# Optimization experiments

Hardware: AMD Instinct MI355X
Metric: run time of the kernel (lower is better)

## Reference

```python
import jax, jax.numpy as jnp
import numpy as np

B, S, D = 2, 2048, 1024
H, HD = 16, 64  # num_heads, head_dim
EPS = 1e-6      # flax LayerNorm default
ROPE_BASE = 10000.0


def _layernorm(x, scale, bias=None, eps=EPS):
    mu = jnp.mean(x, axis=-1, keepdims=True)
    var = jnp.mean(jnp.square(x - mu), axis=-1, keepdims=True)
    y = (x - mu) * jax.lax.rsqrt(var + eps) * scale
    return y + bias if bias is not None else y


def _rotate_half(x):
    x1, x2 = x[..., : x.shape[-1] // 2], x[..., x.shape[-1] // 2 :]
    return jnp.concatenate((-x2, x1), axis=-1)


def _rope_tables(seq_len, head_dim, dtype):
    inv_freq = 1.0 / ROPE_BASE ** (jnp.arange(0, head_dim, 2, dtype=jnp.float32) / head_dim)
    t = jnp.arange(seq_len, dtype=jnp.float32)
    freqs = jnp.einsum('i,j->ij', t, inv_freq)          # [S, HD/2]
    emb = jnp.concatenate((freqs, freqs), axis=-1)      # [S, HD]
    return jnp.cos(emb).astype(dtype), jnp.sin(emb).astype(dtype)


def setup_inputs() -> dict:
    key = jax.random.key(0)
    ks = jax.random.split(key, 4)
    return {
        'x': jax.random.normal(ks[0], (B, S, D), dtype=jnp.float32),
        'w_qkv': jax.random.normal(ks[1], (D, 3 * D), dtype=jnp.float32) * (1.0 / np.sqrt(D)),
        'b_qkv': jnp.zeros((3 * D,), dtype=jnp.float32),
        'w_out': jax.random.normal(ks[2], (D, D), dtype=jnp.float32) * (0.1 / np.sqrt(D)),
        'b_out': jnp.zeros((D,), dtype=jnp.float32),
        'ln_scale': jnp.ones((D,), dtype=jnp.float32),
        'ln_bias': jnp.zeros((D,), dtype=jnp.float32),
        'q_scale': jnp.ones((HD,), dtype=jnp.float32),
        'k_scale': jnp.ones((HD,), dtype=jnp.float32),
    }


def reference(x, w_qkv, b_qkv, w_out, b_out, ln_scale, ln_bias, q_scale, k_scale):
    b, s, d = x.shape
    # input LayerNorm
    xn = _layernorm(x, ln_scale, ln_bias)
    # fused QKV projection
    qkv = xn @ w_qkv + b_qkv                              # [B, S, 3D]
    q, k, v = jnp.split(qkv, 3, axis=-1)
    def to_bhsd(t):
        return t.reshape(b, s, H, HD).transpose(0, 2, 1, 3)
    q, k, v = to_bhsd(q), to_bhsd(k), to_bhsd(v)          # [B, H, S, HD]
    # per-head QK LayerNorm (no bias)
    q = _layernorm(q, q_scale)
    k = _layernorm(k, k_scale)
    # RoPE
    cos, sin = _rope_tables(s, HD, q.dtype)               # [S, HD]
    cos, sin = cos[None, None], sin[None, None]
    q = q * cos + _rotate_half(q) * sin
    k = k * cos + _rotate_half(k) * sin
    # scaled dot-product attention (softmax over key positions)
    scale = 1.0 / np.sqrt(HD)
    scores = jnp.einsum('bhqd,bhkd->bhqk', q, k) * scale  # [B, H, S, S]
    probs = jax.nn.softmax(scores, axis=-1)
    attn = jnp.einsum('bhqk,bhkd->bhqd', probs, v)        # [B, H, S, HD]
    attn = attn.transpose(0, 2, 1, 3).reshape(b, s, d)
    return attn @ w_out + b_out
```

## Files before the change

kernel.cpp:

```cpp
#include <hip/hip_runtime.h>
#include <math.h>

#define BB 2
#define SS 2048
#define DD 1024
#define HH 16
#define HDD 64
static constexpr float EPS = 1e-6f;

typedef __bf16 bf16x8 __attribute__((ext_vector_type(8)));
typedef __bf16 bf16x4 __attribute__((ext_vector_type(4)));
typedef float f32x4 __attribute__((ext_vector_type(4)));
typedef __attribute__((address_space(1))) const unsigned int gas_u32;
typedef __attribute__((address_space(3))) unsigned int las_u32;

__device__ __forceinline__ unsigned short f2bf(float f) {
    unsigned int u = __float_as_uint(f);
    u = (u + 0x7FFFu + ((u >> 16) & 1u)) >> 16;
    return (unsigned short)u;
}

__device__ __forceinline__ uint2 pack4bf(float a, float b, float c, float d) {
    bf16x4 v;
    v[0] = (__bf16)a; v[1] = (__bf16)b; v[2] = (__bf16)c; v[3] = (__bf16)d;
    return *(uint2*)&v;
}

__device__ __forceinline__ void async_ld16(const unsigned short* g, unsigned short* l) {
    __builtin_amdgcn_global_load_lds((gas_u32*)g, (las_u32*)l, 16, 0, 0);
}

__global__ __launch_bounds__(256) void cast_transpose(const float* __restrict__ w,
                                                      unsigned short* __restrict__ wt,
                                                      int K, int N) {
    __shared__ float tile[32][36];
    const int n0 = blockIdx.x * 32;
    const int k0 = blockIdx.y * 32;
    const int t = threadIdx.x;
    const int r = t >> 3;
    const int c = (t & 7) * 4;
    *(float4*)&tile[r][c] = *(const float4*)(w + (size_t)(k0 + r) * N + n0 + c);
    __syncthreads();
    unsigned short o[4];
#pragma unroll
    for (int i = 0; i < 4; i++) o[i] = f2bf(tile[c + i][r]);
    *(uint2*)(wt + (size_t)(n0 + r) * K + k0 + c) = *(uint2*)o;
}

__global__ __launch_bounds__(256) void rope_tables(float* __restrict__ ctab,
                                                   float* __restrict__ stab) {
    const int idx = blockIdx.x * 256 + threadIdx.x;
    const int s = idx >> 5;
    const int i = idx & 31;
    const float ang = (float)s * exp2f(-(float)i * (13.287712379549449f / 32.f));
    ctab[idx] = cosf(ang);
    stab[idx] = sinf(ang);
}

__global__ __launch_bounds__(256) void ln_kernel(const float* __restrict__ x,
                                                 const float* __restrict__ scale,
                                                 const float* __restrict__ bias,
                                                 unsigned short* __restrict__ xn) {
    __shared__ float red[4];
    const int row = blockIdx.x;
    const int t = threadIdx.x;
    const float* xr = x + (size_t)row * DD + t * 4;

    float4 v = *(const float4*)xr;
    float s = v.x + v.y + v.z + v.w;
#pragma unroll
    for (int o = 32; o; o >>= 1) s += __shfl_xor(s, o);
    if ((t & 63) == 0) red[t >> 6] = s;
    __syncthreads();
    const float mu = (red[0] + red[1] + red[2] + red[3]) * (1.f / DD);

    float4 d = {v.x - mu, v.y - mu, v.z - mu, v.w - mu};
    float sq = d.x * d.x + d.y * d.y + d.z * d.z + d.w * d.w;
#pragma unroll
    for (int o = 32; o; o >>= 1) sq += __shfl_xor(sq, o);
    __syncthreads();
    if ((t & 63) == 0) red[t >> 6] = sq;
    __syncthreads();
    const float var = (red[0] + red[1] + red[2] + red[3]) * (1.f / DD);
    const float rstd = rsqrtf(var + EPS);

    const float4 sc = *(const float4*)(scale + t * 4);
    const float4 bi = *(const float4*)(bias + t * 4);
    unsigned short o[4];
    o[0] = f2bf(d.x * rstd * sc.x + bi.x);
    o[1] = f2bf(d.y * rstd * sc.y + bi.y);
    o[2] = f2bf(d.z * rstd * sc.z + bi.z);
    o[3] = f2bf(d.w * rstd * sc.w + bi.w);
    *(uint2*)(xn + (size_t)row * DD + t * 4) = *(uint2*)o;
}

__global__ __launch_bounds__(256) void gemm_mfma_bt(const unsigned short* __restrict__ A,
                                                    const unsigned short* __restrict__ Bt,
                                                    const float* __restrict__ bias,
                                                    float* __restrict__ C,
                                                    int M, int N, int K) {
    __shared__ __align__(16) unsigned short As[128][32];
    __shared__ __align__(16) unsigned short Bs[128][32];

    const int bm = blockIdx.y * 128;
    const int bn = blockIdx.x * 128;
    const int t = threadIdx.x;
    const int wv = t >> 6;
    const int ln = t & 63;
    const int m16 = ln & 15;
    const int quad = ln >> 4;
    const int wm = (wv >> 1) * 64;
    const int wn = (wv & 1) * 64;

    f32x4 acc[4][4];
#pragma unroll
    for (int i = 0; i < 4; i++)
#pragma unroll
        for (int j = 0; j < 4; j++) acc[i][j] = (f32x4){0.f, 0.f, 0.f, 0.f};

    const int srow = wv * 32 + (ln >> 2);
    const int sk = (ln & 3) * 8;
    const unsigned short* aptr = A + (size_t)(bm + srow) * K + sk;
    const unsigned short* bptr = Bt + (size_t)(bn + srow) * K + sk;
    unsigned short* al0 = &As[wv * 32][0];
    unsigned short* al1 = &As[wv * 32 + 16][0];
    unsigned short* bl0 = &Bs[wv * 32][0];
    unsigned short* bl1 = &Bs[wv * 32 + 16][0];

    for (int k0 = 0; k0 < K; k0 += 32) {
        __syncthreads();
        async_ld16(aptr, al0);
        async_ld16(aptr + 16 * (size_t)K, al1);
        async_ld16(bptr, bl0);
        async_ld16(bptr + 16 * (size_t)K, bl1);
        __syncthreads();

        bf16x8 af[4], bf[4];
#pragma unroll
        for (int i = 0; i < 4; i++)
            af[i] = *(const bf16x8*)&As[wm + i * 16 + m16][quad * 8];
#pragma unroll
        for (int j = 0; j < 4; j++)
            bf[j] = *(const bf16x8*)&Bs[wn + j * 16 + m16][quad * 8];
#pragma unroll
        for (int i = 0; i < 4; i++)
#pragma unroll
            for (int j = 0; j < 4; j++)
                acc[i][j] = __builtin_amdgcn_mfma_f32_16x16x32_bf16(af[i], bf[j], acc[i][j], 0, 0, 0);

        aptr += 32;
        bptr += 32;
    }

#pragma unroll
    for (int j = 0; j < 4; j++) {
        const int n = bn + wn + j * 16 + m16;
        const float bv = bias[n];
#pragma unroll
        for (int i = 0; i < 4; i++) {
            float* cp = C + (size_t)(bm + wm + i * 16 + quad * 4) * N + n;
#pragma unroll
            for (int r = 0; r < 4; r++)
                cp[(size_t)r * N] = acc[i][j][r] + bv;
        }
    }
}

__global__ __launch_bounds__(256) void gemm_qkv_fused(const unsigned short* __restrict__ A,
                                                      const unsigned short* __restrict__ Bt,
                                                      const float* __restrict__ bias,
                                                      const float* __restrict__ q_scale,
                                                      const float* __restrict__ k_scale,
                                                      const float* __restrict__ ctab,
                                                      const float* __restrict__ stab,
                                                      unsigned short* __restrict__ qt,
                                                      unsigned short* __restrict__ kt,
                                                      unsigned short* __restrict__ vt,
                                                      int K) {
    __shared__ __align__(16) unsigned short As[128][32];
    __shared__ __align__(16) unsigned short Bs[128][32];

    const int bm = blockIdx.y * 128;
    const int bn = blockIdx.x * 128;
    const int t = threadIdx.x;
    const int wv = t >> 6;
    const int ln = t & 63;
    const int m16 = ln & 15;
    const int quad = ln >> 4;
    const int wm = (wv >> 1) * 64;
    const int wn = (wv & 1) * 64;

    f32x4 acc[4][4];
#pragma unroll
    for (int i = 0; i < 4; i++)
#pragma unroll
        for (int j = 0; j < 4; j++) acc[i][j] = (f32x4){0.f, 0.f, 0.f, 0.f};

    const int srow = wv * 32 + (ln >> 2);
    const int sk = (ln & 3) * 8;
    const unsigned short* aptr = A + (size_t)(bm + srow) * K + sk;
    const unsigned short* bptr = Bt + (size_t)(bn + srow) * K + sk;
    unsigned short* al0 = &As[wv * 32][0];
    unsigned short* al1 = &As[wv * 32 + 16][0];
    unsigned short* bl0 = &Bs[wv * 32][0];
    unsigned short* bl1 = &Bs[wv * 32 + 16][0];

    for (int k0 = 0; k0 < K; k0 += 32) {
        __syncthreads();
        async_ld16(aptr, al0);
        async_ld16(aptr + 16 * (size_t)K, al1);
        async_ld16(bptr, bl0);
        async_ld16(bptr + 16 * (size_t)K, bl1);
        __syncthreads();

        bf16x8 af[4], bf[4];
#pragma unroll
        for (int i = 0; i < 4; i++)
            af[i] = *(const bf16x8*)&As[wm + i * 16 + m16][quad * 8];
#pragma unroll
        for (int j = 0; j < 4; j++)
            bf[j] = *(const bf16x8*)&Bs[wn + j * 16 + m16][quad * 8];
#pragma unroll
        for (int i = 0; i < 4; i++)
#pragma unroll
            for (int j = 0; j < 4; j++)
                acc[i][j] = __builtin_amdgcn_mfma_f32_16x16x32_bf16(af[i], bf[j], acc[i][j], 0, 0, 0);

        aptr += 32;
        bptr += 32;
    }

    const int type = bn >> 10;
    const int h = ((bn & 1023) + wn) >> 6;
    const int rowbase = bm + wm;

    if (type == 2) {
        float bv[4];
#pragma unroll
        for (int j = 0; j < 4; j++) bv[j] = bias[bn + wn + j * 16 + m16];
#pragma unroll
        for (int i = 0; i < 4; i++) {
#pragma unroll
            for (int r = 0; r < 4; r++) {
                const int R = rowbase + i * 16 + quad * 4 + r;
                const int b_ = R >> 11;
                const int s_ = R & (SS - 1);
                unsigned short* orow =
                    vt + (((size_t)(b_ * HH + h) * SS) + s_) * HDD + m16;
#pragma unroll
                for (int j = 0; j < 4; j++)
                    orow[j * 16] = f2bf(acc[i][j][r] + bv[j]);
            }
        }
    } else {
        const float* scalp = (type == 0) ? q_scale : k_scale;
        const float outscale = (type == 0) ? 0.18033688011112042f : 1.0f;
        unsigned short* dst = (type == 0) ? qt : kt;
        float scl[4], bv[4];
#pragma unroll
        for (int j = 0; j < 4; j++) {
            scl[j] = scalp[j * 16 + m16];
            bv[j] = bias[bn + wn + j * 16 + m16];
        }
#pragma unroll
        for (int i = 0; i < 4; i++) {
#pragma unroll
            for (int r = 0; r < 4; r++) {
                const int R = rowbase + i * 16 + quad * 4 + r;
                const int b_ = R >> 11;
                const int s_ = R & (SS - 1);
                float v0 = acc[i][0][r] + bv[0];
                float v1 = acc[i][1][r] + bv[1];
                float v2 = acc[i][2][r] + bv[2];
                float v3 = acc[i][3][r] + bv[3];
                float sm = v0 + v1 + v2 + v3;
                sm += __shfl_xor(sm, 1);
                sm += __shfl_xor(sm, 2);
                sm += __shfl_xor(sm, 4);
                sm += __shfl_xor(sm, 8);
                const float mu = sm * (1.f / 64.f);
                v0 -= mu; v1 -= mu; v2 -= mu; v3 -= mu;
                float sq = v0 * v0 + v1 * v1 + v2 * v2 + v3 * v3;
                sq += __shfl_xor(sq, 1);
                sq += __shfl_xor(sq, 2);
                sq += __shfl_xor(sq, 4);
                sq += __shfl_xor(sq, 8);
                const float rstd = rsqrtf(sq * (1.f / 64.f) + EPS);
                v0 *= rstd * scl[0];
                v1 *= rstd * scl[1];
                v2 *= rstd * scl[2];
                v3 *= rstd * scl[3];
                const float c0 = ctab[s_ * 32 + m16];
                const float s0 = stab[s_ * 32 + m16];
                const float c1 = ctab[s_ * 32 + 16 + m16];
                const float s1 = stab[s_ * 32 + 16 + m16];
                const float o0 = (v0 * c0 - v2 * s0) * outscale;
                const float o1 = (v1 * c1 - v3 * s1) * outscale;
                const float o2 = (v2 * c0 + v0 * s0) * outscale;
                const float o3 = (v3 * c1 + v1 * s1) * outscale;
                unsigned short* orow =
                    dst + (((size_t)(b_ * HH + h) * SS) + s_) * HDD + m16;
                orow[0]  = f2bf(o0);
                orow[16] = f2bf(o1);
                orow[32] = f2bf(o2);
                orow[48] = f2bf(o3);
            }
        }
    }
}

__global__ __launch_bounds__(256) void transpose_v(const unsigned short* __restrict__ vt,
                                                   unsigned short* __restrict__ vtT) {
    __shared__ unsigned short tile[64][72];
    const int bh = blockIdx.x >> 5;
    const int s0 = (blockIdx.x & 31) * 64;
    const int t = threadIdx.x;
    const int row = t >> 2;
    const int c0 = (t & 3) * 16;
    const unsigned short* src = vt + ((size_t)bh * SS + s0 + row) * HDD + c0;
    *(uint4*)&tile[row][c0]     = *(const uint4*)(src);
    *(uint4*)&tile[row][c0 + 8] = *(const uint4*)(src + 8);
    __syncthreads();
    unsigned short outv[16];
#pragma unroll
    for (int i = 0; i < 16; i++) outv[i] = tile[c0 + i][row];
    unsigned short* dst = vtT + ((size_t)bh * HDD + row) * SS + s0 + c0;
    *(uint4*)dst       = *(uint4*)&outv[0];
    *(uint4*)(dst + 8) = *(uint4*)&outv[8];
}

__global__ __launch_bounds__(256, 4) void attn_mfma(const unsigned short* __restrict__ qt,
                                                    const unsigned short* __restrict__ kt,
                                                    const unsigned short* __restrict__ vtT,
                                                    float* __restrict__ Opart,
                                                    float* __restrict__ lpart) {
    __shared__ __align__(16) unsigned short KsS[64 * 64];
    __shared__ __align__(16) unsigned short VsS[64 * 64];
    __shared__ __align__(16) unsigned short PbS[4][32 * 64];

    const int bh = blockIdx.x >> 4;
    const int q0 = (blockIdx.x & 15) * 128;
    const int ks = blockIdx.y;
    const int t = threadIdx.x;
    const int wq = t >> 6;
    const int lane = t & 63;
    const int m16 = lane & 15;
    const int quad = lane >> 4;
    const int m7 = m16 & 7;

    const int cs = quad ^ m7;
    const int koff = m16 * 64 + cs * 8;
    const int srow = t >> 2;
    const int sch = (t & 3) * 2;
    const int sw0 = srow * 64 + ((sch)     ^ (srow & 7)) * 8;
    const int sw1 = srow * 64 + ((sch + 1) ^ (srow & 7)) * 8;
    const int pwb = m16 * 64 + 4 * (quad & 1);
    const int qh = quad >> 1;

    bf16x8 qb[2][2];
#pragma unroll
    for (int u = 0; u < 2; u++) {
        const unsigned short* qp =
            qt + ((size_t)bh * SS + q0 + wq * 32 + u * 16 + m16) * HDD + quad * 8;
        qb[u][0] = *(const bf16x8*)qp;
        qb[u][1] = *(const bf16x8*)(qp + 32);
    }

    bf16x8 ones;
#pragma unroll
    for (int j = 0; j < 8; j++) ones[j] = (__bf16)1.0f;

    f32x4 O[2][4];
#pragma unroll
    for (int u = 0; u < 2; u++)
#pragma unroll
        for (int f = 0; f < 4; f++) O[u][f] = (f32x4){0.f, 0.f, 0.f, 0.f};
    f32x4 lacc[2] = {(f32x4){0.f, 0.f, 0.f, 0.f}, (f32x4){0.f, 0.f, 0.f, 0.f}};

    const unsigned short* kbase = kt + (size_t)bh * SS * HDD;
    const unsigned short* vbase = vtT + (size_t)bh * HDD * SS;
    const f32x4 cinit = (f32x4){-12.f, -12.f, -12.f, -12.f};

    const int kstart = ks * (SS / 2);
    const int kend = kstart + SS / 2;

    uint4 kr0, kr1, vr0, vr1;
    {
        const unsigned short* ksrc = kbase + (size_t)(kstart + srow) * HDD + sch * 8;
        const unsigned short* vsrc = vbase + (size_t)srow * SS + kstart + sch * 8;
        kr0 = *(const uint4*)ksrc;
        kr1 = *(const uint4*)(ksrc + 8);
        vr0 = *(const uint4*)vsrc;
        vr1 = *(const uint4*)(vsrc + 8);
    }

    for (int k0 = kstart; k0 < kend; k0 += 64) {
        __syncthreads();
        *(uint4*)&KsS[sw0] = kr0;
        *(uint4*)&KsS[sw1] = kr1;
        *(uint4*)&VsS[sw0] = vr0;
        *(uint4*)&VsS[sw1] = vr1;
        __syncthreads();

        f32x4 S[2][4];
        __builtin_amdgcn_s_setprio(1);
#pragma unroll
        for (int g = 0; g < 4; g++) {
            const bf16x8 ka0 = *(const bf16x8*)&KsS[g * 1024 + koff];
            const bf16x8 ka1 = *(const bf16x8*)&KsS[g * 1024 + (koff ^ 32)];
#pragma unroll
            for (int u = 0; u < 2; u++) {
                f32x4 a = __builtin_amdgcn_mfma_f32_16x16x32_bf16(ka0, qb[u][0], cinit, 0, 0, 0);
                a = __builtin_amdgcn_mfma_f32_16x16x32_bf16(ka1, qb[u][1], a, 0, 0, 0);
                S[u][g] = a;
            }
        }
        __builtin_amdgcn_s_setprio(0);

#pragma unroll
        for (int u = 0; u < 2; u++) {
#pragma unroll
            for (int g = 0; g < 4; g++) {
                const float p0 = exp2f(S[u][g][0]);
                const float p1 = exp2f(S[u][g][1]);
                const float p2 = exp2f(S[u][g][2]);
                const float p3 = exp2f(S[u][g][3]);
                *(uint2*)&PbS[wq][u * 1024 + pwb + ((2 * g + qh) ^ m7) * 8] =
                    pack4bf(p0, p1, p2, p3);
            }
        }

        if (k0 + 64 < kend) {
            const unsigned short* ksrc = kbase + (size_t)(k0 + 64 + srow) * HDD + sch * 8;
            const unsigned short* vsrc = vbase + (size_t)srow * SS + (k0 + 64) + sch * 8;
            kr0 = *(const uint4*)ksrc;
            kr1 = *(const uint4*)(ksrc + 8);
            vr0 = *(const uint4*)vsrc;
            vr1 = *(const uint4*)(vsrc + 8);
        }

        asm volatile("s_waitcnt lgkmcnt(0)" ::: "memory");

        bf16x8 pb[2][2];
#pragma unroll
        for (int u = 0; u < 2; u++) {
            pb[u][0] = *(const bf16x8*)&PbS[wq][u * 1024 + koff];
            pb[u][1] = *(const bf16x8*)&PbS[wq][u * 1024 + (koff ^ 32)];
        }

        __builtin_amdgcn_s_setprio(1);
#pragma unroll
        for (int u = 0; u < 2; u++) {
            lacc[u] = __builtin_amdgcn_mfma_f32_16x16x32_bf16(ones, pb[u][0], lacc[u], 0, 0, 0);
            lacc[u] = __builtin_amdgcn_mfma_f32_16x16x32_bf16(ones, pb[u][1], lacc[u], 0, 0, 0);
        }
#pragma unroll
        for (int f = 0; f < 4; f++) {
            const bf16x8 va0 = *(const bf16x8*)&VsS[f * 1024 + koff];
            const bf16x8 va1 = *(const bf16x8*)&VsS[f * 1024 + (koff ^ 32)];
#pragma unroll
            for (int u = 0; u < 2; u++) {
                O[u][f] = __builtin_amdgcn_mfma_f32_16x16x32_bf16(va0, pb[u][0], O[u][f], 0, 0, 0);
                O[u][f] = __builtin_amdgcn_mfma_f32_16x16x32_bf16(va1, pb[u][1], O[u][f], 0, 0, 0);
            }
        }
        __builtin_amdgcn_s_setprio(0);
    }

    const int b_ = bh >> 4;
    const int h_ = bh & 15;
    float* obase0 = Opart + (size_t)ks * ((size_t)BB * SS * DD);
#pragma unroll
    for (int u = 0; u < 2; u++) {
        const int s_ = q0 + wq * 32 + u * 16 + m16;
        float* orow = obase0 + ((size_t)b_ * SS + s_) * DD + h_ * HDD;
#pragma unroll
        for (int f = 0; f < 4; f++)
            *(f32x4*)(orow + f * 16 + quad * 4) = O[u][f];
        if (quad == 0)
            lpart[ks * (32 * SS) + bh * SS + s_] = lacc[u][0];
    }
}

__global__ __launch_bounds__(256) void combine_attn(const float* __restrict__ Opart,
                                                    const float* __restrict__ lpart,
                                                    unsigned short* __restrict__ attn) {
    const int row = blockIdx.x;
    const int t = threadIdx.x;
    const int c = t * 4;
    const int h = t >> 4;
    const int b = row >> 11;
    const int s = row & (SS - 1);

    const size_t off = (size_t)row * DD + c;
    const float4 o0 = *(const float4*)(Opart + off);
    const float4 o1 = *(const float4*)(Opart + (size_t)BB * SS * DD + off);
    const int li = (b * HH + h) * SS + s;
    const float inv = 1.f / (lpart[li] + lpart[32 * SS + li]);

    *(uint2*)(attn + off) = pack4bf((o0.x + o1.x) * inv, (o0.y + o1.y) * inv,
                                    (o0.z + o1.z) * inv, (o0.w + o1.w) * inv);
}

extern "C" void kernel_launch(void* const* d_in, const int* in_sizes, int n_in,
                              void* d_out, int out_size, void* d_ws, size_t ws_size,
                              hipStream_t stream) {
    const float* x        = (const float*)d_in[0];
    const float* w_qkv    = (const float*)d_in[1];
    const float* b_qkv    = (const float*)d_in[2];
    const float* w_out    = (const float*)d_in[3];
    const float* b_out    = (const float*)d_in[4];
    const float* ln_scale = (const float*)d_in[5];
    const float* ln_bias  = (const float*)d_in[6];
    const float* q_scale  = (const float*)d_in[7];
    const float* k_scale  = (const float*)d_in[8];
    float* out = (float*)d_out;

    char* ws = (char*)d_ws;
    const size_t MB = 1024 * 1024;
    unsigned short* xn    = (unsigned short*)(ws + 0);
    float*          lpart = (float*)(ws + 8 * MB);
    float*          ctab  = (float*)(ws + 9 * MB);
    float*          stab  = (float*)(ws + 10 * MB);
    float*          Opart = (float*)(ws + 16 * MB);
    unsigned short* wqkvT = (unsigned short*)(ws + 64 * MB);
    unsigned short* woutT = (unsigned short*)(ws + 70 * MB);
    unsigned short* qt    = (unsigned short*)(ws + 72 * MB);
    unsigned short* kt    = (unsigned short*)(ws + 80 * MB);
    unsigned short* vt    = (unsigned short*)(ws + 88 * MB);
    unsigned short* vtT   = (unsigned short*)(ws + 96 * MB);
    unsigned short* attn  = (unsigned short*)(ws + 104 * MB);

    const int M = BB * SS;

    cast_transpose<<<dim3(3 * DD / 32, DD / 32), 256, 0, stream>>>(w_qkv, wqkvT, DD, 3 * DD);
    cast_transpose<<<dim3(DD / 32, DD / 32), 256, 0, stream>>>(w_out, woutT, DD, DD);
    rope_tables<<<SS * 32 / 256, 256, 0, stream>>>(ctab, stab);

    ln_kernel<<<M, 256, 0, stream>>>(x, ln_scale, ln_bias, xn);

    gemm_qkv_fused<<<dim3(3 * DD / 128, M / 128), 256, 0, stream>>>(
        xn, wqkvT, b_qkv, q_scale, k_scale, ctab, stab, qt, kt, vt, DD);

    transpose_v<<<BB * HH * (SS / 64), 256, 0, stream>>>(vt, vtT);

    attn_mfma<<<dim3(BB * HH * (SS / 128), 2), 256, 0, stream>>>(qt, kt, vtT, Opart, lpart);

    combine_attn<<<M, 256, 0, stream>>>(Opart, lpart, attn);

    gemm_mfma_bt<<<dim3(DD / 128, M / 128), 256, 0, stream>>>(attn, woutT, b_out, out,
                                                              M, DD, DD);
}
```

Baseline: 266.2 us.

## Drop split-K attention and fuse normalization into attention epilogue with block swizzle

Removes the two-way key split in the attention kernel so each block processes all keys and normalizes its output directly, writing bf16 attention output. This eliminates the fp32 partial output buffers and the separate combine kernel, saving a launch and roughly 32MB of intermediate traffic. It also remaps block indices with a swizzle so that consecutive blocks spread across heads. The cost is half as many blocks (512), which lowers parallelism and lengthens each block's serial loop.

```diff
diff --git a/kernel.cpp b/kernel.cpp
--- a/kernel.cpp
+++ b/kernel.cpp
@@ -332,15 +332,15 @@
 __global__ __launch_bounds__(256, 4) void attn_mfma(const unsigned short* __restrict__ qt,
                                                     const unsigned short* __restrict__ kt,
                                                     const unsigned short* __restrict__ vtT,
-                                                    float* __restrict__ Opart,
-                                                    float* __restrict__ lpart) {
+                                                    unsigned short* __restrict__ attn) {
     __shared__ __align__(16) unsigned short KsS[64 * 64];
     __shared__ __align__(16) unsigned short VsS[64 * 64];
     __shared__ __align__(16) unsigned short PbS[4][32 * 64];
 
-    const int bh = blockIdx.x >> 4;
-    const int q0 = (blockIdx.x & 15) * 128;
-    const int ks = blockIdx.y;
+    const int bid = blockIdx.x;
+    const int swz = (bid & 7) * 64 + (bid >> 3);
+    const int bh = swz >> 4;
+    const int q0 = (swz & 15) * 128;
     const int t = threadIdx.x;
     const int wq = t >> 6;
     const int lane = t & 63;
@@ -381,20 +381,17 @@
     const unsigned short* vbase = vtT + (size_t)bh * HDD * SS;
     const f32x4 cinit = (f32x4){-12.f, -12.f, -12.f, -12.f};
 
-    const int kstart = ks * (SS / 2);
-    const int kend = kstart + SS / 2;
-
     uint4 kr0, kr1, vr0, vr1;
     {
-        const unsigned short* ksrc = kbase + (size_t)(kstart + srow) * HDD + sch * 8;
-        const unsigned short* vsrc = vbase + (size_t)srow * SS + kstart + sch * 8;
+        const unsigned short* ksrc = kbase + (size_t)srow * HDD + sch * 8;
+        const unsigned short* vsrc = vbase + (size_t)srow * SS + sch * 8;
         kr0 = *(const uint4*)ksrc;
         kr1 = *(const uint4*)(ksrc + 8);
         vr0 = *(const uint4*)vsrc;
         vr1 = *(const uint4*)(vsrc + 8);
     }
 
-    for (int k0 = kstart; k0 < kend; k0 += 64) {
+    for (int k0 = 0; k0 < SS; k0 += 64) {
         __syncthreads();
         *(uint4*)&KsS[sw0] = kr0;
         *(uint4*)&KsS[sw1] = kr1;
@@ -430,7 +427,7 @@
             }
         }
 
-        if (k0 + 64 < kend) {
+        if (k0 + 64 < SS) {
             const unsigned short* ksrc = kbase + (size_t)(k0 + 64 + srow) * HDD + sch * 8;
             const unsigned short* vsrc = vbase + (size_t)srow * SS + (k0 + 64) + sch * 8;
             kr0 = *(const uint4*)ksrc;
@@ -469,37 +466,17 @@
 
     const int b_ = bh >> 4;
     const int h_ = bh & 15;
-    float* obase0 = Opart + (size_t)ks * ((size_t)BB * SS * DD);
 #pragma unroll
     for (int u = 0; u < 2; u++) {
+        const float inv = 1.f / lacc[u][0];
         const int s_ = q0 + wq * 32 + u * 16 + m16;
-        float* orow = obase0 + ((size_t)b_ * SS + s_) * DD + h_ * HDD;
+        unsigned short* orow = attn + ((size_t)b_ * SS + s_) * DD + h_ * HDD;
 #pragma unroll
         for (int f = 0; f < 4; f++)
-            *(f32x4*)(orow + f * 16 + quad * 4) = O[u][f];
-        if (quad == 0)
-            lpart[ks * (32 * SS) + bh * SS + s_] = lacc[u][0];
-    }
-}
-
-__global__ __launch_bounds__(256) void combine_attn(const float* __restrict__ Opart,
-                                                    const float* __restrict__ lpart,
-                                                    unsigned short* __restrict__ attn) {
-    const int row = blockIdx.x;
-    const int t = threadIdx.x;
-    const int c = t * 4;
-    const int h = t >> 4;
-    const int b = row >> 11;
-    const int s = row & (SS - 1);
-
-    const size_t off = (size_t)row * DD + c;
-    const float4 o0 = *(const float4*)(Opart + off);
-    const float4 o1 = *(const float4*)(Opart + (size_t)BB * SS * DD + off);
-    const int li = (b * HH + h) * SS + s;
-    const float inv = 1.f / (lpart[li] + lpart[32 * SS + li]);
-
-    *(uint2*)(attn + off) = pack4bf((o0.x + o1.x) * inv, (o0.y + o1.y) * inv,
-                                    (o0.z + o1.z) * inv, (o0.w + o1.w) * inv);
+            *(uint2*)(orow + f * 16 + quad * 4) =
+                pack4bf(O[u][f][0] * inv, O[u][f][1] * inv,
+                        O[u][f][2] * inv, O[u][f][3] * inv);
+    }
 }
 
 extern "C" void kernel_launch(void* const* d_in, const int* in_sizes, int n_in,
@@ -519,10 +496,8 @@
     char* ws = (char*)d_ws;
     const size_t MB = 1024 * 1024;
     unsigned short* xn    = (unsigned short*)(ws + 0);
-    float*          lpart = (float*)(ws + 8 * MB);
     float*          ctab  = (float*)(ws + 9 * MB);
     float*          stab  = (float*)(ws + 10 * MB);
-    float*          Opart = (float*)(ws + 16 * MB);
     unsigned short* wqkvT = (unsigned short*)(ws + 64 * MB);
     unsigned short* woutT = (unsigned short*)(ws + 70 * MB);
     unsigned short* qt    = (unsigned short*)(ws + 72 * MB);
@@ -544,9 +519,7 @@
 
     transpose_v<<<BB * HH * (SS / 64), 256, 0, stream>>>(vt, vtT);
 
-    attn_mfma<<<dim3(BB * HH * (SS / 128), 2), 256, 0, stream>>>(qt, kt, vtT, Opart, lpart);
-
-    combine_attn<<<M, 256, 0, stream>>>(Opart, lpart, attn);
+    attn_mfma<<<dim3(BB * HH * (SS / 128)), 256, 0, stream>>>(qt, kt, vtT, attn);
 
     gemm_mfma_bt<<<dim3(DD / 128, M / 128), 256, 0, stream>>>(attn, woutT, b_out, out,
                                                               M, DD, DD);
```

Measured after the change: 265.4 us. Within noise of the previous version (-0.3%).
